# Kernel tuning notes

Measured on AMD Instinct MI355X. Metric: run time of the kernel, lower is better.

The kernel has to match this reference:

```python
import jax, jax.numpy as jnp
import numpy as np


def setup_inputs() -> dict:
    key = jax.random.key(0)
    ks = jax.random.split(key, 8)
    B, Cin, H, W = 32, 4, 512, 512
    Cout, Cred = 3, 2
    x = jax.random.normal(ks[0], (B, Cin, H, W), dtype=jnp.float32)
    # channel attention params (1x1 convs == linear on channels)
    ca_w1 = jax.random.normal(ks[1], (Cred, Cin), dtype=jnp.float32) * 0.1
    ca_b1 = jnp.zeros((Cred,), dtype=jnp.float32)
    ca_w2 = jax.random.normal(ks[2], (Cin, Cred), dtype=jnp.float32) * 0.1
    ca_b2 = jnp.zeros((Cin,), dtype=jnp.float32)
    # main 1x1 conv, initialized as in _init_weights: eye on first 3x3, small noise on NIR column
    conv_w = np.zeros((Cout, Cin), dtype=np.float32)
    conv_w[:3, :3] = np.eye(3, dtype=np.float32)
    conv_w[:, 3:] = 0.01 * np.asarray(jax.random.normal(ks[3], (Cout, Cin - 3)))
    conv_w = jnp.asarray(conv_w)
    conv_b = jnp.zeros((Cout,), dtype=jnp.float32)
    # spatial attention 7x7 conv: [out=1, in=Cout, 7, 7]
    sa_w = jax.random.normal(ks[4], (1, Cout, 7, 7), dtype=jnp.float32) * 0.05
    sa_b = jnp.zeros((1,), dtype=jnp.float32)
    return {"x": x, "ca_w1": ca_w1, "ca_b1": ca_b1, "ca_w2": ca_w2, "ca_b2": ca_b2,
            "conv_w": conv_w, "conv_b": conv_b, "sa_w": sa_w, "sa_b": sa_b}


def reference(x, ca_w1, ca_b1, ca_w2, ca_b2, conv_w, conv_b, sa_w, sa_b):
    # x: [B, Cin, H, W]
    # Channel attention: global avg pool -> 1x1 conv -> relu -> 1x1 conv -> sigmoid
    pooled = jnp.mean(x, axis=(2, 3))                      # [B, Cin]
    h = jax.nn.relu(jnp.einsum('rc,bc->br', ca_w1, pooled) + ca_b1)   # [B, Cred]
    att = jax.nn.sigmoid(jnp.einsum('cr,br->bc', ca_w2, h) + ca_b2)   # [B, Cin]
    x_weighted = x * att[:, :, None, None]                 # [B, Cin, H, W]
    # 1x1 conv to Cout
    out = jnp.einsum('oc,bchw->bohw', conv_w, x_weighted) + conv_b[None, :, None, None]
    # Spatial attention: 7x7 conv -> sigmoid -> gate
    sp = jax.lax.conv_general_dilated(
        out, sa_w, window_strides=(1, 1), padding=((3, 3), (3, 3)),
        dimension_numbers=('NCHW', 'OIHW', 'NCHW'))        # [B, 1, H, W]
    spatial_att = jax.nn.sigmoid(sp + sa_b[None, :, None, None])
    return out * spatial_att
```

## Files before the change

### kernel.cpp

```cpp
#include <hip/hip_runtime.h>
#include <math.h>
#include <stdint.h>

#define HW (512*512)
#define TSX 128
#define TSY 32
#define NROW 38
#define NQ 34
#define LSTRH 68
#define CHS (NROW*LSTRH)

typedef __fp16 h2 __attribute__((ext_vector_type(2)));

__device__ __forceinline__ h2 u2h(uint32_t u) { union { uint32_t u; h2 h; } c; c.u = u; return c.h; }
__device__ __forceinline__ uint32_t h2u(h2 h) { union { h2 h; uint32_t u; } c; c.h = h; return c.u; }

#if __has_builtin(__builtin_amdgcn_fdot2)
#define FDOT2(a, b, c) __builtin_amdgcn_fdot2((a), (b), (c), false)
#else
__device__ __forceinline__ float fdot2_asm(h2 a, h2 b, float c) {
    float d;
    asm("v_dot2_f32_f16 %0, %1, %2, %3" : "=v"(d) : "v"(a), "v"(b), "v"(c));
    return d;
}
#define FDOT2(a, b, c) fdot2_asm((a), (b), (c))
#endif

__global__ __launch_bounds__(256) void k_reduce(const float* __restrict__ x,
                                                float* __restrict__ ws) {
    int bid = blockIdx.x;
    int plane = bid >> 3, j = bid & 7;
    const float4* xv = (const float4*)x + (size_t)plane * 65536 + (size_t)j * 8192;
    int tid = threadIdx.x;
    float s = 0.f;
    #pragma unroll
    for (int k = 0; k < 32; ++k) {
        float4 v = xv[(size_t)k * 256 + tid];
        s += (v.x + v.y) + (v.z + v.w);
    }
    #pragma unroll
    for (int off = 32; off > 0; off >>= 1) s += __shfl_down(s, off, 64);
    __shared__ float red[4];
    if ((tid & 63) == 0) red[tid >> 6] = s;
    __syncthreads();
    if (tid == 0) ws[bid] = (red[0] + red[1]) + (red[2] + red[3]);
}

__global__ __launch_bounds__(128) void k_mlp(const float* __restrict__ part,
                                             const float* __restrict__ w1,
                                             const float* __restrict__ b1,
                                             const float* __restrict__ w2,
                                             const float* __restrict__ b2,
                                             float* __restrict__ att_out) {
    __shared__ float pool[128];
    __shared__ float hbuf[64];
    int tid = threadIdx.x;
    float s = 0.f;
    #pragma unroll
    for (int j = 0; j < 8; ++j) s += part[tid * 8 + j];
    pool[tid] = s * (1.f / 262144.f);
    __syncthreads();
    if (tid < 64) {
        int b = tid >> 1, r = tid & 1;
        float h = b1[r];
        #pragma unroll
        for (int c = 0; c < 4; ++c) h += w1[r * 4 + c] * pool[b * 4 + c];
        hbuf[tid] = fmaxf(h, 0.f);
    }
    __syncthreads();
    {
        int b = tid >> 2, c = tid & 3;
        float z = b2[c];
        #pragma unroll
        for (int r = 0; r < 2; ++r) z += w2[c * 2 + r] * hbuf[b * 2 + r];
        att_out[tid] = 1.f / (1.f + __expf(-z));
    }
}

__global__ __launch_bounds__(256, 5) void k_fused(const float* __restrict__ x,
                                                  const float* __restrict__ conv_w,
                                                  const float* __restrict__ conv_b,
                                                  const float* __restrict__ sa_w,
                                                  const float* __restrict__ sa_b,
                                                  const float* __restrict__ att,
                                                  float* __restrict__ out) {
    __shared__ uint32_t s_pre[3 * CHS];
    int tid = threadIdx.x;
    int b = blockIdx.z;
    int ty0 = blockIdx.y * TSY, tx0 = blockIdx.x * TSX;

    float kw[12], kb[3];
    #pragma unroll
    for (int t = 0; t < 12; ++t) kw[t] = conv_w[t] * att[b * 4 + (t & 3)];
    #pragma unroll
    for (int o = 0; o < 3; ++o) kb[o] = conv_b[o];
    float sbias = sa_b[0];
    const float* xb = x + (size_t)b * 4 * HW;

    for (int u = tid; u < NROW * NQ; u += 256) {
        int r = u / NQ, q = u - r * NQ;
        int gy = ty0 - 3 + r;
        int gx0 = tx0 - 4 + q * 4;
        float4 o0 = make_float4(0.f, 0.f, 0.f, 0.f), o1 = o0, o2 = o0;
        if ((unsigned)gy < 512u && (unsigned)gx0 <= 508u) {
            size_t off = (size_t)gy * 512 + gx0;
            float4 X0 = *(const float4*)(xb + off);
            float4 X1 = *(const float4*)(xb + HW + off);
            float4 X2 = *(const float4*)(xb + 2 * HW + off);
            float4 X3 = *(const float4*)(xb + 3 * HW + off);
#define DO1(comp) \
            o0.comp = kb[0] + kw[0]*X0.comp + kw[1]*X1.comp + kw[2]*X2.comp + kw[3]*X3.comp; \
            o1.comp = kb[1] + kw[4]*X0.comp + kw[5]*X1.comp + kw[6]*X2.comp + kw[7]*X3.comp; \
            o2.comp = kb[2] + kw[8]*X0.comp + kw[9]*X1.comp + kw[10]*X2.comp + kw[11]*X3.comp;
            DO1(x) DO1(y) DO1(z) DO1(w)
#undef DO1
        }
        int base = r * LSTRH + 2 * q;
        *(uint2*)(&s_pre[base]) = make_uint2(h2u(__builtin_amdgcn_cvt_pkrtz(o0.x, o0.y)),
                                             h2u(__builtin_amdgcn_cvt_pkrtz(o0.z, o0.w)));
        *(uint2*)(&s_pre[base + CHS]) = make_uint2(h2u(__builtin_amdgcn_cvt_pkrtz(o1.x, o1.y)),
                                                   h2u(__builtin_amdgcn_cvt_pkrtz(o1.z, o1.w)));
        *(uint2*)(&s_pre[base + 2 * CHS]) = make_uint2(h2u(__builtin_amdgcn_cvt_pkrtz(o2.x, o2.y)),
                                                       h2u(__builtin_amdgcn_cvt_pkrtz(o2.z, o2.w)));
    }
    __syncthreads();

    int txi = tid & 15, tyr = tid >> 4;
    float acc[2][8];
    #pragma unroll
    for (int i = 0; i < 2; ++i)
        #pragma unroll
        for (int j = 0; j < 8; ++j) acc[i][j] = 0.f;

    #pragma clang loop unroll(disable)
    for (int ch = 0; ch < 3; ++ch) {
        const uint32_t* sbp = &s_pre[ch * CHS];
        uint32_t pw[7][4];
        #pragma unroll
        for (int dy = 0; dy < 7; ++dy) {
            const float* wr = sa_w + ch * 49 + dy * 7;
            pw[dy][0] = h2u(__builtin_amdgcn_cvt_pkrtz(wr[0], wr[1]));
            pw[dy][1] = h2u(__builtin_amdgcn_cvt_pkrtz(wr[2], wr[3]));
            pw[dy][2] = h2u(__builtin_amdgcn_cvt_pkrtz(wr[4], wr[5]));
            pw[dy][3] = h2u(__builtin_amdgcn_cvt_pkrtz(wr[6], 0.f));
        }
        #pragma unroll
        for (int k = 0; k < 8; ++k) {
            int lr = 2 * tyr + k;
            const uint32_t* rowp = sbp + lr * LSTRH + 4 * txi;
            uint4 ra = *(const uint4*)(rowp);
            uint4 rb = *(const uint4*)(rowp + 4);
            uint32_t r_[8] = {ra.x, ra.y, ra.z, ra.w, rb.x, rb.y, rb.z, rb.w};
            uint32_t pr[15];
            #pragma unroll
            for (int m = 0; m < 8; ++m) pr[2 * m < 15 ? 2 * m : 0] = r_[m];
            #pragma unroll
            for (int m = 0; m < 7; ++m)
                pr[2 * m + 1] = __builtin_amdgcn_alignbit(r_[m + 1], r_[m], 16);
            #pragma unroll
            for (int i = 0; i < 2; ++i) {
                int dy = k - i;
                if (dy >= 0 && dy <= 6) {
                    h2 w01 = u2h(pw[dy][0]);
                    h2 w23 = u2h(pw[dy][1]);
                    h2 w45 = u2h(pw[dy][2]);
                    h2 w6z = u2h(pw[dy][3]);
                    #pragma unroll
                    for (int j = 0; j < 8; ++j) {
                        float a = acc[i][j];
                        a = FDOT2(w01, u2h(pr[j + 1]), a);
                        a = FDOT2(w23, u2h(pr[j + 3]), a);
                        a = FDOT2(w45, u2h(pr[j + 5]), a);
                        a = FDOT2(w6z, u2h(pr[j + 7]), a);
                        acc[i][j] = a;
                    }
                }
            }
        }
    }

    float* ob = out + (size_t)b * 3 * HW;
    #pragma unroll
    for (int i = 0; i < 2; ++i) {
        float g[8];
        #pragma unroll
        for (int j = 0; j < 8; ++j) g[j] = 1.f / (1.f + __expf(-(acc[i][j] + sbias)));
        int lr = 2 * tyr + 3 + i;
        size_t off = (size_t)(ty0 + 2 * tyr + i) * 512 + (tx0 + 8 * txi);
        #pragma unroll
        for (int ch = 0; ch < 3; ++ch) {
            const uint32_t* cp = &s_pre[ch * CHS + lr * LSTRH + 4 * txi + 2];
            uint2 ca = *(const uint2*)(cp);
            uint2 cb = *(const uint2*)(cp + 2);
            h2 c0 = u2h(ca.x), c1 = u2h(ca.y), c2 = u2h(cb.x), c3 = u2h(cb.y);
            float4 A, B;
            A.x = (float)c0.x * g[0]; A.y = (float)c0.y * g[1];
            A.z = (float)c1.x * g[2]; A.w = (float)c1.y * g[3];
            B.x = (float)c2.x * g[4]; B.y = (float)c2.y * g[5];
            B.z = (float)c3.x * g[6]; B.w = (float)c3.y * g[7];
            *(float4*)(ob + (size_t)ch * HW + off)     = A;
            *(float4*)(ob + (size_t)ch * HW + off + 4) = B;
        }
    }
}

extern "C" void kernel_launch(void* const* d_in, const int* in_sizes, int n_in,
                              void* d_out, int out_size, void* d_ws, size_t ws_size,
                              hipStream_t stream) {
    const float* x      = (const float*)d_in[0];
    const float* ca_w1  = (const float*)d_in[1];
    const float* ca_b1  = (const float*)d_in[2];
    const float* ca_w2  = (const float*)d_in[3];
    const float* ca_b2  = (const float*)d_in[4];
    const float* conv_w = (const float*)d_in[5];
    const float* conv_b = (const float*)d_in[6];
    const float* sa_w   = (const float*)d_in[7];
    const float* sa_b   = (const float*)d_in[8];
    float* ws  = (float*)d_ws;
    float* out = (float*)d_out;

    hipLaunchKernelGGL(k_reduce, dim3(1024), dim3(256), 0, stream, x, ws);
    hipLaunchKernelGGL(k_mlp, dim3(1), dim3(128), 0, stream,
                       ws, ca_w1, ca_b1, ca_w2, ca_b2, ws + 1024);
    hipLaunchKernelGGL(k_fused, dim3(512 / TSX, 512 / TSY, 32), dim3(256), 0, stream,
                       x, conv_w, conv_b, sa_w, sa_b, ws + 1024, out);
}
```

Before: 91.27 us.

## Batch global loads in staging and drop alignbit shifts via even/odd weight packing

The staging loop is split into two unrolled batches of three items, so all twelve float4 global loads in a batch are issued before any arithmetic. This is meant to raise memory-level parallelism. The conv inner loop now uses two packed-weight sets, one for even outputs (shifted, with a leading zero) and one for odd outputs. These let dot2 read the LDS words directly and remove the per-row alignbit instructions. The cost is more live registers for the prefetched data and the doubled weight arrays, which may lower occupancy.

```diff
diff --git a/kernel.cpp b/kernel.cpp
--- a/kernel.cpp
+++ b/kernel.cpp
@@ -9,6 +9,7 @@
 #define NQ 34
 #define LSTRH 68
 #define CHS (NROW*LSTRH)
+#define NITEMS (NROW*NQ)
 
 typedef __fp16 h2 __attribute__((ext_vector_type(2)));
 
@@ -97,32 +98,81 @@
     float sbias = sa_b[0];
     const float* xb = x + (size_t)b * 4 * HW;
 
-    for (int u = tid; u < NROW * NQ; u += 256) {
-        int r = u / NQ, q = u - r * NQ;
-        int gy = ty0 - 3 + r;
-        int gx0 = tx0 - 4 + q * 4;
-        float4 o0 = make_float4(0.f, 0.f, 0.f, 0.f), o1 = o0, o2 = o0;
-        if ((unsigned)gy < 512u && (unsigned)gx0 <= 508u) {
-            size_t off = (size_t)gy * 512 + gx0;
-            float4 X0 = *(const float4*)(xb + off);
-            float4 X1 = *(const float4*)(xb + HW + off);
-            float4 X2 = *(const float4*)(xb + 2 * HW + off);
-            float4 X3 = *(const float4*)(xb + 3 * HW + off);
-#define DO1(comp) \
-            o0.comp = kb[0] + kw[0]*X0.comp + kw[1]*X1.comp + kw[2]*X2.comp + kw[3]*X3.comp; \
-            o1.comp = kb[1] + kw[4]*X0.comp + kw[5]*X1.comp + kw[6]*X2.comp + kw[7]*X3.comp; \
-            o2.comp = kb[2] + kw[8]*X0.comp + kw[9]*X1.comp + kw[10]*X2.comp + kw[11]*X3.comp;
-            DO1(x) DO1(y) DO1(z) DO1(w)
-#undef DO1
-        }
-        int base = r * LSTRH + 2 * q;
-        *(uint2*)(&s_pre[base]) = make_uint2(h2u(__builtin_amdgcn_cvt_pkrtz(o0.x, o0.y)),
-                                             h2u(__builtin_amdgcn_cvt_pkrtz(o0.z, o0.w)));
-        *(uint2*)(&s_pre[base + CHS]) = make_uint2(h2u(__builtin_amdgcn_cvt_pkrtz(o1.x, o1.y)),
-                                                   h2u(__builtin_amdgcn_cvt_pkrtz(o1.z, o1.w)));
-        *(uint2*)(&s_pre[base + 2 * CHS]) = make_uint2(h2u(__builtin_amdgcn_cvt_pkrtz(o2.x, o2.y)),
-                                                       h2u(__builtin_amdgcn_cvt_pkrtz(o2.z, o2.w)));
-    }
+#define GATEWRITE(Xs, inb_, r_, q_)                                                   \
+    {                                                                                 \
+        float4 o0 = make_float4(0.f,0.f,0.f,0.f), o1 = o0, o2 = o0;                   \
+        if (inb_) {                                                                   \
+            float4 X0 = Xs[0], X1 = Xs[1], X2 = Xs[2], X3 = Xs[3];                    \
+            o0.x = kb[0] + kw[0]*X0.x + kw[1]*X1.x + kw[2]*X2.x + kw[3]*X3.x;         \
+            o0.y = kb[0] + kw[0]*X0.y + kw[1]*X1.y + kw[2]*X2.y + kw[3]*X3.y;         \
+            o0.z = kb[0] + kw[0]*X0.z + kw[1]*X1.z + kw[2]*X2.z + kw[3]*X3.z;         \
+            o0.w = kb[0] + kw[0]*X0.w + kw[1]*X1.w + kw[2]*X2.w + kw[3]*X3.w;         \
+            o1.x = kb[1] + kw[4]*X0.x + kw[5]*X1.x + kw[6]*X2.x + kw[7]*X3.x;         \
+            o1.y = kb[1] + kw[4]*X0.y + kw[5]*X1.y + kw[6]*X2.y + kw[7]*X3.y;         \
+            o1.z = kb[1] + kw[4]*X0.z + kw[5]*X1.z + kw[6]*X2.z + kw[7]*X3.z;         \
+            o1.w = kb[1] + kw[4]*X0.w + kw[5]*X1.w + kw[6]*X2.w + kw[7]*X3.w;         \
+            o2.x = kb[2] + kw[8]*X0.x + kw[9]*X1.x + kw[10]*X2.x + kw[11]*X3.x;       \
+            o2.y = kb[2] + kw[8]*X0.y + kw[9]*X1.y + kw[10]*X2.y + kw[11]*X3.y;       \
+            o2.z = kb[2] + kw[8]*X0.z + kw[9]*X1.z + kw[10]*X2.z + kw[11]*X3.z;       \
+            o2.w = kb[2] + kw[8]*X0.w + kw[9]*X1.w + kw[10]*X2.w + kw[11]*X3.w;       \
+        }                                                                             \
+        int base_ = (r_) * LSTRH + 2 * (q_);                                          \
+        *(uint2*)(&s_pre[base_]) = make_uint2(h2u(__builtin_amdgcn_cvt_pkrtz(o0.x, o0.y)),  \
+                                              h2u(__builtin_amdgcn_cvt_pkrtz(o0.z, o0.w))); \
+        *(uint2*)(&s_pre[base_ + CHS]) = make_uint2(h2u(__builtin_amdgcn_cvt_pkrtz(o1.x, o1.y)),  \
+                                                    h2u(__builtin_amdgcn_cvt_pkrtz(o1.z, o1.w))); \
+        *(uint2*)(&s_pre[base_ + 2*CHS]) = make_uint2(h2u(__builtin_amdgcn_cvt_pkrtz(o2.x, o2.y)),  \
+                                                      h2u(__builtin_amdgcn_cvt_pkrtz(o2.z, o2.w))); \
+    }
+
+    {
+        float4 Xa[3][4]; bool va[3]; int ra[3], qa[3];
+        #pragma unroll
+        for (int t = 0; t < 3; ++t) {
+            int u = tid + t * 256;
+            int r = u / NQ, q = u - r * NQ;
+            int gy = ty0 - 3 + r, gx0 = tx0 - 4 + q * 4;
+            bool inb = ((unsigned)gy < 512u) && ((unsigned)gx0 <= 508u);
+            ra[t] = r; qa[t] = q; va[t] = inb;
+            float4 z = make_float4(0.f,0.f,0.f,0.f);
+            Xa[t][0] = z; Xa[t][1] = z; Xa[t][2] = z; Xa[t][3] = z;
+            if (inb) {
+                size_t off = (size_t)gy * 512 + gx0;
+                Xa[t][0] = *(const float4*)(xb + off);
+                Xa[t][1] = *(const float4*)(xb + HW + off);
+                Xa[t][2] = *(const float4*)(xb + 2 * HW + off);
+                Xa[t][3] = *(const float4*)(xb + 3 * HW + off);
+            }
+        }
+        #pragma unroll
+        for (int t = 0; t < 3; ++t) GATEWRITE(Xa[t], va[t], ra[t], qa[t])
+    }
+    {
+        float4 Xa[3][4]; bool va[3]; int ra[3], qa[3]; bool lv[3];
+        #pragma unroll
+        for (int t = 0; t < 3; ++t) {
+            int u = tid + (t + 3) * 256;
+            bool lim = (u < NITEMS);
+            lv[t] = lim;
+            int uc = lim ? u : 0;
+            int r = uc / NQ, q = uc - r * NQ;
+            int gy = ty0 - 3 + r, gx0 = tx0 - 4 + q * 4;
+            bool inb = lim && ((unsigned)gy < 512u) && ((unsigned)gx0 <= 508u);
+            ra[t] = r; qa[t] = q; va[t] = inb;
+            float4 z = make_float4(0.f,0.f,0.f,0.f);
+            Xa[t][0] = z; Xa[t][1] = z; Xa[t][2] = z; Xa[t][3] = z;
+            if (inb) {
+                size_t off = (size_t)gy * 512 + gx0;
+                Xa[t][0] = *(const float4*)(xb + off);
+                Xa[t][1] = *(const float4*)(xb + HW + off);
+                Xa[t][2] = *(const float4*)(xb + 2 * HW + off);
+                Xa[t][3] = *(const float4*)(xb + 3 * HW + off);
+            }
+        }
+        #pragma unroll
+        for (int t = 0; t < 3; ++t) if (lv[t]) GATEWRITE(Xa[t], va[t], ra[t], qa[t])
+    }
+#undef GATEWRITE
     __syncthreads();
 
     int txi = tid & 15, tyr = tid >> 4;
@@ -135,14 +185,18 @@
     #pragma clang loop unroll(disable)
     for (int ch = 0; ch < 3; ++ch) {
         const uint32_t* sbp = &s_pre[ch * CHS];
-        uint32_t pw[7][4];
+        uint32_t pwE[7][4], pwO[7][4];
         #pragma unroll
         for (int dy = 0; dy < 7; ++dy) {
             const float* wr = sa_w + ch * 49 + dy * 7;
-            pw[dy][0] = h2u(__builtin_amdgcn_cvt_pkrtz(wr[0], wr[1]));
-            pw[dy][1] = h2u(__builtin_amdgcn_cvt_pkrtz(wr[2], wr[3]));
-            pw[dy][2] = h2u(__builtin_amdgcn_cvt_pkrtz(wr[4], wr[5]));
-            pw[dy][3] = h2u(__builtin_amdgcn_cvt_pkrtz(wr[6], 0.f));
+            pwE[dy][0] = h2u(__builtin_amdgcn_cvt_pkrtz(0.f,   wr[0]));
+            pwE[dy][1] = h2u(__builtin_amdgcn_cvt_pkrtz(wr[1], wr[2]));
+            pwE[dy][2] = h2u(__builtin_amdgcn_cvt_pkrtz(wr[3], wr[4]));
+            pwE[dy][3] = h2u(__builtin_amdgcn_cvt_pkrtz(wr[5], wr[6]));
+            pwO[dy][0] = h2u(__builtin_amdgcn_cvt_pkrtz(wr[0], wr[1]));
+            pwO[dy][1] = h2u(__builtin_amdgcn_cvt_pkrtz(wr[2], wr[3]));
+            pwO[dy][2] = h2u(__builtin_amdgcn_cvt_pkrtz(wr[4], wr[5]));
+            pwO[dy][3] = h2u(__builtin_amdgcn_cvt_pkrtz(wr[6], 0.f));
         }
         #pragma unroll
         for (int k = 0; k < 8; ++k) {
@@ -151,28 +205,19 @@
             uint4 ra = *(const uint4*)(rowp);
             uint4 rb = *(const uint4*)(rowp + 4);
             uint32_t r_[8] = {ra.x, ra.y, ra.z, ra.w, rb.x, rb.y, rb.z, rb.w};
-            uint32_t pr[15];
-            #pragma unroll
-            for (int m = 0; m < 8; ++m) pr[2 * m < 15 ? 2 * m : 0] = r_[m];
-            #pragma unroll
-            for (int m = 0; m < 7; ++m)
-                pr[2 * m + 1] = __builtin_amdgcn_alignbit(r_[m + 1], r_[m], 16);
             #pragma unroll
             for (int i = 0; i < 2; ++i) {
                 int dy = k - i;
                 if (dy >= 0 && dy <= 6) {
-                    h2 w01 = u2h(pw[dy][0]);
-                    h2 w23 = u2h(pw[dy][1]);
-                    h2 w45 = u2h(pw[dy][2]);
-                    h2 w6z = u2h(pw[dy][3]);
                     #pragma unroll
-                    for (int j = 0; j < 8; ++j) {
-                        float a = acc[i][j];
-                        a = FDOT2(w01, u2h(pr[j + 1]), a);
-                        a = FDOT2(w23, u2h(pr[j + 3]), a);
-                        a = FDOT2(w45, u2h(pr[j + 5]), a);
-                        a = FDOT2(w6z, u2h(pr[j + 7]), a);
-                        acc[i][j] = a;
+                    for (int jh = 0; jh < 4; ++jh) {
+                        float aE = acc[i][2 * jh], aO = acc[i][2 * jh + 1];
+                        #pragma unroll
+                        for (int p = 0; p < 4; ++p) {
+                            aE = FDOT2(u2h(pwE[dy][p]), u2h(r_[jh + p]), aE);
+                            aO = FDOT2(u2h(pwO[dy][p]), u2h(r_[jh + p + 1]), aO);
+                        }
+                        acc[i][2 * jh] = aE; acc[i][2 * jh + 1] = aO;
                     }
                 }
             }
```

Result: faster. 81.77 us (-10.4%).

## Halve spatial tile height, prepack 7x7 weights in MLP kernel, batch halo loads

Applied to the files above, without the earlier changes.

Cuts the fused kernel tile from 32 to 16 rows so each thread computes one output row instead of two, and raises the launch-bounds occupancy hint from 5 to 8 blocks. The 7x7 attention weights are converted to packed fp16 pairs once in the MLP kernel, with even and odd shifted copies, which removes the per-block conversion and alignbit shuffles. Halo loads are issued for all three items first and computed afterwards, exposing more memory parallelism. Centre values are kept in registers from the conv pass rather than re-read from LDS. The cost is more halo overhead per output (22 loaded rows for 16 output rows instead of 38 for 32) and twice as many blocks.

```diff
diff --git a/kernel.cpp b/kernel.cpp
--- a/kernel.cpp
+++ b/kernel.cpp
@@ -4,11 +4,12 @@
 
 #define HW (512*512)
 #define TSX 128
-#define TSY 32
-#define NROW 38
+#define TSY 16
+#define NROW 22
 #define NQ 34
 #define LSTRH 68
 #define CHS (NROW*LSTRH)
+#define NITEMS (NROW*NQ)
 
 typedef __fp16 h2 __attribute__((ext_vector_type(2)));
 
@@ -46,19 +47,33 @@
     if (tid == 0) ws[bid] = (red[0] + red[1]) + (red[2] + red[3]);
 }
 
-__global__ __launch_bounds__(128) void k_mlp(const float* __restrict__ part,
+__global__ __launch_bounds__(256) void k_mlp(const float* __restrict__ part,
                                              const float* __restrict__ w1,
                                              const float* __restrict__ b1,
                                              const float* __restrict__ w2,
                                              const float* __restrict__ b2,
+                                             const float* __restrict__ sa_w,
                                              float* __restrict__ att_out) {
     __shared__ float pool[128];
     __shared__ float hbuf[64];
     int tid = threadIdx.x;
-    float s = 0.f;
-    #pragma unroll
-    for (int j = 0; j < 8; ++j) s += part[tid * 8 + j];
-    pool[tid] = s * (1.f / 262144.f);
+
+    if (tid < 168) {
+        int ch = tid / 56, rest = tid - ch * 56;
+        int dy = rest >> 3, p = rest & 7;
+        const float* wr = sa_w + ch * 49 + dy * 7;
+        float a, c;
+        if (p < 4) { a = (p == 0) ? 0.f : wr[2 * p - 1]; c = wr[2 * p]; }
+        else       { int pp = p - 4; a = wr[2 * pp]; c = (pp == 3) ? 0.f : wr[2 * pp + 1]; }
+        ((uint32_t*)att_out)[128 + tid] = h2u(__builtin_amdgcn_cvt_pkrtz(a, c));
+    }
+
+    if (tid < 128) {
+        float s = 0.f;
+        #pragma unroll
+        for (int j = 0; j < 8; ++j) s += part[tid * 8 + j];
+        pool[tid] = s * (1.f / 262144.f);
+    }
     __syncthreads();
     if (tid < 64) {
         int b = tid >> 1, r = tid & 1;
@@ -68,7 +83,7 @@
         hbuf[tid] = fmaxf(h, 0.f);
     }
     __syncthreads();
-    {
+    if (tid < 128) {
         int b = tid >> 2, c = tid & 3;
         float z = b2[c];
         #pragma unroll
@@ -77,10 +92,10 @@
     }
 }
 
-__global__ __launch_bounds__(256, 5) void k_fused(const float* __restrict__ x,
+__global__ __launch_bounds__(256, 8) void k_fused(const float* __restrict__ x,
                                                   const float* __restrict__ conv_w,
                                                   const float* __restrict__ conv_b,
-                                                  const float* __restrict__ sa_w,
+                                                  const uint32_t* __restrict__ wpk,
                                                   const float* __restrict__ sa_b,
                                                   const float* __restrict__ att,
                                                   float* __restrict__ out) {
@@ -97,110 +112,103 @@
     float sbias = sa_b[0];
     const float* xb = x + (size_t)b * 4 * HW;
 
-    for (int u = tid; u < NROW * NQ; u += 256) {
-        int r = u / NQ, q = u - r * NQ;
-        int gy = ty0 - 3 + r;
-        int gx0 = tx0 - 4 + q * 4;
-        float4 o0 = make_float4(0.f, 0.f, 0.f, 0.f), o1 = o0, o2 = o0;
-        if ((unsigned)gy < 512u && (unsigned)gx0 <= 508u) {
-            size_t off = (size_t)gy * 512 + gx0;
-            float4 X0 = *(const float4*)(xb + off);
-            float4 X1 = *(const float4*)(xb + HW + off);
-            float4 X2 = *(const float4*)(xb + 2 * HW + off);
-            float4 X3 = *(const float4*)(xb + 3 * HW + off);
+    {
+        float4 Xa[3][4]; bool va[3], lv[3]; int ra[3], qa[3];
+        #pragma unroll
+        for (int t = 0; t < 3; ++t) {
+            int u = tid + t * 256;
+            bool lim = (u < NITEMS);
+            lv[t] = lim;
+            int uc = lim ? u : 0;
+            int r = uc / NQ, q = uc - r * NQ;
+            int gy = ty0 - 3 + r, gx0 = tx0 - 4 + q * 4;
+            bool inb = lim && ((unsigned)gy < 512u) && ((unsigned)gx0 <= 508u);
+            ra[t] = r; qa[t] = q; va[t] = inb;
+            float4 z = make_float4(0.f, 0.f, 0.f, 0.f);
+            Xa[t][0] = z; Xa[t][1] = z; Xa[t][2] = z; Xa[t][3] = z;
+            if (inb) {
+                size_t off = (size_t)gy * 512 + gx0;
+                Xa[t][0] = *(const float4*)(xb + off);
+                Xa[t][1] = *(const float4*)(xb + HW + off);
+                Xa[t][2] = *(const float4*)(xb + 2 * HW + off);
+                Xa[t][3] = *(const float4*)(xb + 3 * HW + off);
+            }
+        }
+        #pragma unroll
+        for (int t = 0; t < 3; ++t) {
+            if (!lv[t]) continue;
+            float4 X0 = Xa[t][0], X1 = Xa[t][1], X2 = Xa[t][2], X3 = Xa[t][3];
+            float4 o0 = make_float4(0.f,0.f,0.f,0.f), o1 = o0, o2 = o0;
+            if (va[t]) {
 #define DO1(comp) \
-            o0.comp = kb[0] + kw[0]*X0.comp + kw[1]*X1.comp + kw[2]*X2.comp + kw[3]*X3.comp; \
-            o1.comp = kb[1] + kw[4]*X0.comp + kw[5]*X1.comp + kw[6]*X2.comp + kw[7]*X3.comp; \
-            o2.comp = kb[2] + kw[8]*X0.comp + kw[9]*X1.comp + kw[10]*X2.comp + kw[11]*X3.comp;
-            DO1(x) DO1(y) DO1(z) DO1(w)
+                o0.comp = kb[0] + kw[0]*X0.comp + kw[1]*X1.comp + kw[2]*X2.comp + kw[3]*X3.comp; \
+                o1.comp = kb[1] + kw[4]*X0.comp + kw[5]*X1.comp + kw[6]*X2.comp + kw[7]*X3.comp; \
+                o2.comp = kb[2] + kw[8]*X0.comp + kw[9]*X1.comp + kw[10]*X2.comp + kw[11]*X3.comp;
+                DO1(x) DO1(y) DO1(z) DO1(w)
 #undef DO1
+            }
+            int base = ra[t] * LSTRH + 2 * qa[t];
+            *(uint2*)(&s_pre[base]) = make_uint2(h2u(__builtin_amdgcn_cvt_pkrtz(o0.x, o0.y)),
+                                                 h2u(__builtin_amdgcn_cvt_pkrtz(o0.z, o0.w)));
+            *(uint2*)(&s_pre[base + CHS]) = make_uint2(h2u(__builtin_amdgcn_cvt_pkrtz(o1.x, o1.y)),
+                                                       h2u(__builtin_amdgcn_cvt_pkrtz(o1.z, o1.w)));
+            *(uint2*)(&s_pre[base + 2 * CHS]) = make_uint2(h2u(__builtin_amdgcn_cvt_pkrtz(o2.x, o2.y)),
+                                                           h2u(__builtin_amdgcn_cvt_pkrtz(o2.z, o2.w)));
         }
-        int base = r * LSTRH + 2 * q;
-        *(uint2*)(&s_pre[base]) = make_uint2(h2u(__builtin_amdgcn_cvt_pkrtz(o0.x, o0.y)),
-                                             h2u(__builtin_amdgcn_cvt_pkrtz(o0.z, o0.w)));
-        *(uint2*)(&s_pre[base + CHS]) = make_uint2(h2u(__builtin_amdgcn_cvt_pkrtz(o1.x, o1.y)),
-                                                   h2u(__builtin_amdgcn_cvt_pkrtz(o1.z, o1.w)));
-        *(uint2*)(&s_pre[base + 2 * CHS]) = make_uint2(h2u(__builtin_amdgcn_cvt_pkrtz(o2.x, o2.y)),
-                                                       h2u(__builtin_amdgcn_cvt_pkrtz(o2.z, o2.w)));
     }
     __syncthreads();
 
     int txi = tid & 15, tyr = tid >> 4;
-    float acc[2][8];
-    #pragma unroll
-    for (int i = 0; i < 2; ++i)
-        #pragma unroll
-        for (int j = 0; j < 8; ++j) acc[i][j] = 0.f;
+    float acc[8];
+    #pragma unroll
+    for (int j = 0; j < 8; ++j) acc[j] = 0.f;
+    uint2 ctr[3];
+    uint2 ctr2[3];
 
     #pragma clang loop unroll(disable)
     for (int ch = 0; ch < 3; ++ch) {
         const uint32_t* sbp = &s_pre[ch * CHS];
-        uint32_t pw[7][4];
-        #pragma unroll
-        for (int dy = 0; dy < 7; ++dy) {
-            const float* wr = sa_w + ch * 49 + dy * 7;
-            pw[dy][0] = h2u(__builtin_amdgcn_cvt_pkrtz(wr[0], wr[1]));
-            pw[dy][1] = h2u(__builtin_amdgcn_cvt_pkrtz(wr[2], wr[3]));
-            pw[dy][2] = h2u(__builtin_amdgcn_cvt_pkrtz(wr[4], wr[5]));
-            pw[dy][3] = h2u(__builtin_amdgcn_cvt_pkrtz(wr[6], 0.f));
-        }
-        #pragma unroll
-        for (int k = 0; k < 8; ++k) {
-            int lr = 2 * tyr + k;
+        const uint32_t* wp = wpk + ch * 56;
+        #pragma unroll
+        for (int k = 0; k < 7; ++k) {
+            int lr = tyr + k;
             const uint32_t* rowp = sbp + lr * LSTRH + 4 * txi;
             uint4 ra = *(const uint4*)(rowp);
             uint4 rb = *(const uint4*)(rowp + 4);
             uint32_t r_[8] = {ra.x, ra.y, ra.z, ra.w, rb.x, rb.y, rb.z, rb.w};
-            uint32_t pr[15];
+            if (k == 3) {
+                ctr[ch]  = make_uint2(r_[2], r_[3]);
+                ctr2[ch] = make_uint2(r_[4], r_[5]);
+            }
             #pragma unroll
-            for (int m = 0; m < 8; ++m) pr[2 * m < 15 ? 2 * m : 0] = r_[m];
-            #pragma unroll
-            for (int m = 0; m < 7; ++m)
-                pr[2 * m + 1] = __builtin_amdgcn_alignbit(r_[m + 1], r_[m], 16);
-            #pragma unroll
-            for (int i = 0; i < 2; ++i) {
-                int dy = k - i;
-                if (dy >= 0 && dy <= 6) {
-                    h2 w01 = u2h(pw[dy][0]);
-                    h2 w23 = u2h(pw[dy][1]);
-                    h2 w45 = u2h(pw[dy][2]);
-                    h2 w6z = u2h(pw[dy][3]);
-                    #pragma unroll
-                    for (int j = 0; j < 8; ++j) {
-                        float a = acc[i][j];
-                        a = FDOT2(w01, u2h(pr[j + 1]), a);
-                        a = FDOT2(w23, u2h(pr[j + 3]), a);
-                        a = FDOT2(w45, u2h(pr[j + 5]), a);
-                        a = FDOT2(w6z, u2h(pr[j + 7]), a);
-                        acc[i][j] = a;
-                    }
+            for (int jh = 0; jh < 4; ++jh) {
+                float aE = acc[2 * jh], aO = acc[2 * jh + 1];
+                #pragma unroll
+                for (int p = 0; p < 4; ++p) {
+                    aE = FDOT2(u2h(wp[k * 8 + p]),     u2h(r_[jh + p]),     aE);
+                    aO = FDOT2(u2h(wp[k * 8 + 4 + p]), u2h(r_[jh + p + 1]), aO);
                 }
+                acc[2 * jh] = aE; acc[2 * jh + 1] = aO;
             }
         }
     }
 
+    float g[8];
+    #pragma unroll
+    for (int j = 0; j < 8; ++j) g[j] = 1.f / (1.f + __expf(-(acc[j] + sbias)));
     float* ob = out + (size_t)b * 3 * HW;
-    #pragma unroll
-    for (int i = 0; i < 2; ++i) {
-        float g[8];
-        #pragma unroll
-        for (int j = 0; j < 8; ++j) g[j] = 1.f / (1.f + __expf(-(acc[i][j] + sbias)));
-        int lr = 2 * tyr + 3 + i;
-        size_t off = (size_t)(ty0 + 2 * tyr + i) * 512 + (tx0 + 8 * txi);
-        #pragma unroll
-        for (int ch = 0; ch < 3; ++ch) {
-            const uint32_t* cp = &s_pre[ch * CHS + lr * LSTRH + 4 * txi + 2];
-            uint2 ca = *(const uint2*)(cp);
-            uint2 cb = *(const uint2*)(cp + 2);
-            h2 c0 = u2h(ca.x), c1 = u2h(ca.y), c2 = u2h(cb.x), c3 = u2h(cb.y);
-            float4 A, B;
-            A.x = (float)c0.x * g[0]; A.y = (float)c0.y * g[1];
-            A.z = (float)c1.x * g[2]; A.w = (float)c1.y * g[3];
-            B.x = (float)c2.x * g[4]; B.y = (float)c2.y * g[5];
-            B.z = (float)c3.x * g[6]; B.w = (float)c3.y * g[7];
-            *(float4*)(ob + (size_t)ch * HW + off)     = A;
-            *(float4*)(ob + (size_t)ch * HW + off + 4) = B;
-        }
+    size_t off = (size_t)(ty0 + tyr) * 512 + (tx0 + 8 * txi);
+    #pragma unroll
+    for (int ch = 0; ch < 3; ++ch) {
+        h2 c0 = u2h(ctr[ch].x),  c1 = u2h(ctr[ch].y);
+        h2 c2 = u2h(ctr2[ch].x), c3 = u2h(ctr2[ch].y);
+        float4 A, B;
+        A.x = (float)c0.x * g[0]; A.y = (float)c0.y * g[1];
+        A.z = (float)c1.x * g[2]; A.w = (float)c1.y * g[3];
+        B.x = (float)c2.x * g[4]; B.y = (float)c2.y * g[5];
+        B.z = (float)c3.x * g[6]; B.w = (float)c3.y * g[7];
+        *(float4*)(ob + (size_t)ch * HW + off)     = A;
+        *(float4*)(ob + (size_t)ch * HW + off + 4) = B;
     }
 }
 
@@ -219,9 +227,12 @@
     float* ws  = (float*)d_ws;
     float* out = (float*)d_out;
 
+    float* att = ws + 1024;
+    const uint32_t* wpk = (const uint32_t*)att + 128;
+
     hipLaunchKernelGGL(k_reduce, dim3(1024), dim3(256), 0, stream, x, ws);
-    hipLaunchKernelGGL(k_mlp, dim3(1), dim3(128), 0, stream,
-                       ws, ca_w1, ca_b1, ca_w2, ca_b2, ws + 1024);
+    hipLaunchKernelGGL(k_mlp, dim3(1), dim3(256), 0, stream,
+                       ws, ca_w1, ca_b1, ca_w2, ca_b2, sa_w, att);
     hipLaunchKernelGGL(k_fused, dim3(512 / TSX, 512 / TSY, 32), dim3(256), 0, stream,
-                       x, conv_w, conv_b, sa_w, sa_b, ws + 1024, out);
-}
+                       x, conv_w, conv_b, wpk, sa_b, att, out);
+}
```

Measured after the change: 176.0 us. 92.8% more time.
